# Kernel optimization log

Hardware: AMD Instinct MI355X
Metric: run time of the kernel (lower is better)

Reference implementation:

```python
import jax, jax.numpy as jnp
import numpy as np

T, B, D, H, DFF = 512, 32, 1024, 16, 4096
DK = D // H
SCALE = 1.0 / np.sqrt(DK)
EPS = 1e-5


def _layernorm(x, w, b):
    mu = jnp.mean(x, axis=-1, keepdims=True)
    var = jnp.mean(jnp.square(x - mu), axis=-1, keepdims=True)
    return (x - mu) * jax.lax.rsqrt(var + EPS) * w + b


def _gru_gate(x, y, wg, bg):
    # gates: (..., 3, D) from Linear(2D -> 3D, no bias)
    g = jnp.concatenate([x, y], axis=-1) @ wg.T
    g = g.reshape(*g.shape[:-1], 3, D)
    r = jax.nn.sigmoid(g[..., 0, :])
    z = jax.nn.sigmoid(g[..., 1, :] - bg)
    h = jnp.tanh(g[..., 2, :] * r)
    return (1 - z) * x + z * h


def _attention(x, w_qkv, w_out, b_out):
    t = x.shape[0]
    qkv = (x @ w_qkv.T).reshape(t, -1, 3, H, DK)  # (T,B,3,H,dk)
    q, k, v = qkv[:, :, 0], qkv[:, :, 1], qkv[:, :, 2]  # (T,B,H,dk)
    scores = jnp.einsum('tbhd,sbhd->bhts', q, k) * SCALE
    causal = jnp.triu(jnp.ones((t, t), dtype=bool), k=1)
    scores = jnp.where(causal, -jnp.inf, scores)
    attn = jax.nn.softmax(scores, axis=-1)
    out = jnp.einsum('bhts,sbhd->tbhd', attn, v).reshape(t, -1, D)
    return out @ w_out.T + b_out


def setup_inputs() -> dict:
    key = jax.random.key(0)
    ks = jax.random.split(key, 10)
    s = lambda k, shape, scale: jax.random.normal(k, shape, dtype=jnp.float32) * scale
    return {
        'x': s(ks[0], (T, B, D), 1.0),
        'w_qkv': s(ks[1], (3 * D, D), 0.02),
        'w_out': s(ks[2], (D, D), 0.02),
        'b_out': jnp.zeros((D,), jnp.float32),
        'ln1_w': jnp.ones((D,), jnp.float32),
        'ln1_b': jnp.zeros((D,), jnp.float32),
        'ln2_w': jnp.ones((D,), jnp.float32),
        'ln2_b': jnp.zeros((D,), jnp.float32),
        'w_ff1': s(ks[3], (DFF, D), 0.02),
        'b_ff1': jnp.zeros((DFF,), jnp.float32),
        'w_ff2': s(ks[4], (D, DFF), 0.02),
        'b_ff2': jnp.zeros((D,), jnp.float32),
        'g1_w': s(ks[5], (3 * D, 2 * D), 0.02),
        'g1_bg': jnp.full((D,), 2.0, jnp.float32),
        'g2_w': s(ks[6], (3 * D, 2 * D), 0.02),
        'g2_bg': jnp.full((D,), 2.0, jnp.float32),
    }


def reference(x, w_qkv, w_out, b_out, ln1_w, ln1_b, ln2_w, ln2_b,
              w_ff1, b_ff1, w_ff2, b_ff2, g1_w, g1_bg, g2_w, g2_bg):
    attn_out = _attention(_layernorm(x, ln1_w, ln1_b), w_qkv, w_out, b_out)
    h1 = _gru_gate(x, attn_out, g1_w, g1_bg)
    h = _layernorm(h1, ln2_w, ln2_b)
    ff = jax.nn.relu(h @ w_ff1.T + b_ff1) @ w_ff2.T + b_ff2
    return _gru_gate(h1, ff, g2_w, g2_bg)
```

## Files before the change

kernel.cpp:

```cpp
#include <hip/hip_runtime.h>

#define TT   512
#define BB   32
#define DD   1024
#define HH   16
#define NROW 16384

typedef __attribute__((ext_vector_type(4))) float f32x4;
typedef __attribute__((ext_vector_type(8))) short s16x8;
typedef __attribute__((ext_vector_type(4))) short s16x4;

__device__ __forceinline__ unsigned short f2bf(float f) {
    unsigned int u = __float_as_uint(f);
    u += 0x7fffu + ((u >> 16) & 1u);
    return (unsigned short)(u >> 16);
}
__device__ __forceinline__ float bf2f(unsigned short h) {
    return __uint_as_float(((unsigned int)h) << 16);
}

__device__ __forceinline__ void gload16(const unsigned short* g, unsigned short* l) {
    __builtin_amdgcn_global_load_lds(
        (const __attribute__((address_space(1))) unsigned int*)g,
        (__attribute__((address_space(3))) unsigned int*)l, 16, 0, 0);
}

__global__ __launch_bounds__(256, 8)
void fill_f32(float* __restrict__ p, float v) {
    const size_t i = ((size_t)blockIdx.x * 256 + threadIdx.x) * 4;
    f32x4 o = (f32x4){v, v, v, v};
    *(f32x4*)(p + i) = o;
}

__global__ __launch_bounds__(256, 8)
void cvt_weights(const float* __restrict__ s0, const float* __restrict__ s1,
                 const float* __restrict__ s2, const float* __restrict__ s3,
                 const float* __restrict__ s4, const float* __restrict__ s5,
                 unsigned short* __restrict__ dst) {
    const int i = blockIdx.x * 256 + threadIdx.x;
    const float* src;
    int base;
    if      (i <  786432) { src = s0; base = 0;       }
    else if (i < 1048576) { src = s1; base = 786432;  }
    else if (i < 2097152) { src = s2; base = 1048576; }
    else if (i < 3145728) { src = s3; base = 2097152; }
    else if (i < 4718592) { src = s4; base = 3145728; }
    else                  { src = s5; base = 4718592; }
    f32x4 v = *(const f32x4*)(src + (size_t)(i - base) * 4);
    s16x4 o;
#pragma unroll
    for (int j = 0; j < 4; ++j) o[j] = (short)f2bf(v[j]);
    *(s16x4*)(dst + (size_t)i * 4) = o;
}

__global__ __launch_bounds__(256, 8)
void cvt_rows(const float* __restrict__ in, unsigned short* __restrict__ out, int ld_out) {
    const int row = blockIdx.x;
    const int d   = threadIdx.x * 4;
    f32x4 v = *(const f32x4*)(in + (size_t)row * DD + d);
    s16x4 o;
#pragma unroll
    for (int j = 0; j < 4; ++j) o[j] = (short)f2bf(v[j]);
    *(s16x4*)(out + (size_t)row * ld_out + d) = o;
}

__global__ __launch_bounds__(256, 4)
void ln_fwd(const float* __restrict__ in, const float* __restrict__ w,
            const float* __restrict__ bsh, unsigned short* __restrict__ out,
            unsigned short* __restrict__ side, int ld_side) {
    const int row = blockIdx.x;
    const int tid = threadIdx.x;
    f32x4 v = *(const f32x4*)(in + (size_t)row * DD + tid * 4);
    float s = v[0] + v[1] + v[2] + v[3];
    float q = v[0]*v[0] + v[1]*v[1] + v[2]*v[2] + v[3]*v[3];
#pragma unroll
    for (int d = 1; d < 64; d <<= 1) {
        s += __shfl_xor(s, d, 64);
        q += __shfl_xor(q, d, 64);
    }
    __shared__ float red[8];
    const int lane = tid & 63, wv = tid >> 6;
    if (lane == 0) { red[wv] = s; red[4 + wv] = q; }
    __syncthreads();
    s = red[0] + red[1] + red[2] + red[3];
    q = red[4] + red[5] + red[6] + red[7];
    const float mu   = s * (1.f / 1024.f);
    const float rstd = rsqrtf(q * (1.f / 1024.f) - mu * mu + 1e-5f);
    f32x4 w4 = *(const f32x4*)(w + tid * 4);
    f32x4 b4 = *(const f32x4*)(bsh + tid * 4);
    s16x4 o;
#pragma unroll
    for (int j = 0; j < 4; ++j) o[j] = (short)f2bf((v[j] - mu) * rstd * w4[j] + b4[j]);
    *(s16x4*)(out + (size_t)row * DD + tid * 4) = o;
    if (side) {
        s16x4 sx;
#pragma unroll
        for (int j = 0; j < 4; ++j) sx[j] = (short)f2bf(v[j]);
        *(s16x4*)(side + (size_t)row * ld_side + tid * 4) = sx;
    }
}

__global__ __launch_bounds__(256, 2)
void gemm_bf16(const unsigned short* __restrict__ A,
               const unsigned short* __restrict__ W,
               unsigned short* __restrict__ C,
               const float* __restrict__ bias,
               int M, int N, int K, int ldc, int relu) {
    __shared__ unsigned short lds_a[128 * 64];
    __shared__ unsigned short lds_b[128 * 64];

    const int tid  = threadIdx.x;
    const int lane = tid & 63;
    const int wv   = tid >> 6;
    const int wm   = wv >> 1;
    const int wn   = wv & 1;
    const int m0   = blockIdx.y * 128;
    const int n0   = blockIdx.x * 128;
    const int l15  = lane & 15;
    const int l4   = lane >> 4;
    const int lrow   = lane >> 3;
    const int gchunk = (lane & 7) ^ lrow;

    f32x4 acc[4][4];
#pragma unroll
    for (int i = 0; i < 4; ++i)
#pragma unroll
        for (int j = 0; j < 4; ++j) acc[i][j] = (f32x4){0.f, 0.f, 0.f, 0.f};

    for (int k0 = 0; k0 < K; k0 += 64) {
        __syncthreads();
#pragma unroll
        for (int i = 0; i < 4; ++i) {
            const int r = (wv * 4 + i) * 8 + lrow;
            gload16(A + (size_t)(m0 + r) * K + k0 + gchunk * 8, lds_a + (wv * 4 + i) * 512);
            gload16(W + (size_t)(n0 + r) * K + k0 + gchunk * 8, lds_b + (wv * 4 + i) * 512);
        }
        __syncthreads();
#pragma unroll
        for (int ks = 0; ks < 2; ++ks) {
            s16x8 af[4], bfr[4];
#pragma unroll
            for (int mi = 0; mi < 4; ++mi) {
                const int row = wm * 64 + mi * 16 + l15;
                const int c   = ks * 4 + l4;
                af[mi] = *(const s16x8*)(lds_a + row * 64 + ((c ^ (row & 7)) * 8));
            }
#pragma unroll
            for (int ni = 0; ni < 4; ++ni) {
                const int row = wn * 64 + ni * 16 + l15;
                const int c   = ks * 4 + l4;
                bfr[ni] = *(const s16x8*)(lds_b + row * 64 + ((c ^ (row & 7)) * 8));
            }
#pragma unroll
            for (int mi = 0; mi < 4; ++mi)
#pragma unroll
                for (int ni = 0; ni < 4; ++ni)
                    acc[mi][ni] = __builtin_amdgcn_mfma_f32_16x16x32_bf16(
                        af[mi], bfr[ni], acc[mi][ni], 0, 0, 0);
        }
    }

    const int r0 = l4 * 4;
#pragma unroll
    for (int ni = 0; ni < 4; ++ni) {
        const int col = n0 + wn * 64 + ni * 16 + l15;
        const float bv = bias ? bias[col] : 0.f;
#pragma unroll
        for (int mi = 0; mi < 4; ++mi) {
            const int rowb = m0 + wm * 64 + mi * 16 + r0;
#pragma unroll
            for (int r = 0; r < 4; ++r) {
                float v = acc[mi][ni][r] + bv;
                if (relu) v = fmaxf(v, 0.f);
                C[(size_t)(rowb + r) * ldc + col] = f2bf(v);
            }
        }
    }
}

__global__ __launch_bounds__(256, 2)
void repack_qkv(const unsigned short* __restrict__ qkv,
                unsigned short* __restrict__ Qo, unsigned short* __restrict__ Ko,
                unsigned short* __restrict__ Vt) {
    __shared__ unsigned short vlds[64][65];
    const int tid = threadIdx.x;
    const int t0  = blockIdx.x * 64;
    const int bh  = blockIdx.y;
    const int b   = bh >> 4, h = bh & 15;
    {
        const int row = tid >> 2, ch = tid & 3;
        const int t = t0 + row;
        const unsigned short* src = qkv + (size_t)(t * BB + b) * 3072 + h * 64 + ch * 16;
        const size_t doff = ((size_t)bh * 512 + t) * 64 + ch * 16;
        *(s16x8*)(Qo + doff)     = *(const s16x8*)(src);
        *(s16x8*)(Qo + doff + 8) = *(const s16x8*)(src + 8);
        *(s16x8*)(Ko + doff)     = *(const s16x8*)(src + 1024);
        *(s16x8*)(Ko + doff + 8) = *(const s16x8*)(src + 1032);
    }
#pragma unroll
    for (int it = 0; it < 2; ++it) {
        const int vr = (tid >> 3) + it * 32;
        const int c8 = tid & 7;
        s16x8 val = *(const s16x8*)(qkv + (size_t)((t0 + vr) * BB + b) * 3072 + 2048 + h * 64 + c8 * 8);
#pragma unroll
        for (int j = 0; j < 8; ++j) vlds[vr][c8 * 8 + j] = (unsigned short)val[j];
    }
    __syncthreads();
    {
        const int dk = tid >> 2, ch = tid & 3;
        s16x8 o0, o1;
#pragma unroll
        for (int j = 0; j < 8; ++j) {
            o0[j] = (short)vlds[ch * 16 + j][dk];
            o1[j] = (short)vlds[ch * 16 + 8 + j][dk];
        }
        const size_t doff = ((size_t)bh * 64 + dk) * 512 + t0 + ch * 16;
        *(s16x8*)(Vt + doff)     = o0;
        *(s16x8*)(Vt + doff + 8) = o1;
    }
}

__global__ __launch_bounds__(256, 2)
void attn_fwd(const unsigned short* __restrict__ Qm,
              const unsigned short* __restrict__ Km,
              const unsigned short* __restrict__ Vt,
              unsigned short* __restrict__ Om) {
    __shared__ unsigned short lds_k[64 * 64];
    __shared__ unsigned short lds_v[64 * 64];
    __shared__ unsigned short p_lds[4][16 * 72];

    const int tid  = threadIdx.x;
    const int lane = tid & 63;
    const int wv   = tid >> 6;
    const int q0   = blockIdx.x * 64;
    const int bh   = blockIdx.y;
    const int b    = bh >> 4, h = bh & 15;
    const int l15  = lane & 15;
    const int l4   = lane >> 4;
    const int lrow   = lane >> 3;
    const int gchunk = (lane & 7) ^ lrow;

    s16x8 qa[2];
    {
        const unsigned short* qp = Qm + ((size_t)bh * 512 + q0 + wv * 16 + l15) * 64 + l4 * 8;
        qa[0] = *(const s16x8*)(qp);
        qa[1] = *(const s16x8*)(qp + 32);
    }

    f32x4 oacc[4];
#pragma unroll
    for (int i = 0; i < 4; ++i) oacc[i] = (f32x4){0.f, 0.f, 0.f, 0.f};
    float m_run[4], l_run[4];
#pragma unroll
    for (int r = 0; r < 4; ++r) { m_run[r] = -1e30f; l_run[r] = 0.f; }

    const int rowg0 = q0 + wv * 16 + l4 * 4;

    for (int s0 = 0; s0 <= q0; s0 += 64) {
        __syncthreads();
#pragma unroll
        for (int i = 0; i < 2; ++i) {
            const int r = (wv * 2 + i) * 8 + lrow;
            gload16(Km + ((size_t)bh * 512 + s0 + r) * 64 + gchunk * 8, lds_k + (wv * 2 + i) * 512);
            gload16(Vt + ((size_t)bh * 64 + r) * 512 + s0 + gchunk * 8, lds_v + (wv * 2 + i) * 512);
        }
        __syncthreads();

        float svv[4][4];
#pragma unroll
        for (int ni = 0; ni < 4; ++ni) {
            f32x4 s = (f32x4){0.f, 0.f, 0.f, 0.f};
#pragma unroll
            for (int ks = 0; ks < 2; ++ks) {
                const int row = ni * 16 + l15;
                const int c   = ks * 4 + l4;
                s16x8 kb = *(const s16x8*)(lds_k + row * 64 + ((c ^ (row & 7)) * 8));
                s = __builtin_amdgcn_mfma_f32_16x16x32_bf16(qa[ks], kb, s, 0, 0, 0);
            }
            const int colg = s0 + ni * 16 + l15;
#pragma unroll
            for (int r = 0; r < 4; ++r)
                svv[ni][r] = (colg > rowg0 + r) ? -1e30f : s[r] * 0.125f;
        }
#pragma unroll
        for (int r = 0; r < 4; ++r) {
            float mt = fmaxf(fmaxf(svv[0][r], svv[1][r]), fmaxf(svv[2][r], svv[3][r]));
            mt = fmaxf(mt, __shfl_xor(mt, 1, 64));
            mt = fmaxf(mt, __shfl_xor(mt, 2, 64));
            mt = fmaxf(mt, __shfl_xor(mt, 4, 64));
            mt = fmaxf(mt, __shfl_xor(mt, 8, 64));
            const float mn    = fmaxf(m_run[r], mt);
            const float alpha = __expf(m_run[r] - mn);
            m_run[r] = mn;
            float rs = 0.f;
#pragma unroll
            for (int ni = 0; ni < 4; ++ni) {
                const float p = __expf(svv[ni][r] - mn);
                svv[ni][r] = p;
                rs += p;
            }
            rs += __shfl_xor(rs, 1, 64);
            rs += __shfl_xor(rs, 2, 64);
            rs += __shfl_xor(rs, 4, 64);
            rs += __shfl_xor(rs, 8, 64);
            l_run[r] = l_run[r] * alpha + rs;
#pragma unroll
            for (int ni = 0; ni < 4; ++ni) oacc[ni][r] *= alpha;
        }
#pragma unroll
        for (int ni = 0; ni < 4; ++ni)
#pragma unroll
            for (int r = 0; r < 4; ++r)
                p_lds[wv][(l4 * 4 + r) * 72 + ni * 16 + l15] = f2bf(svv[ni][r]);
        __syncthreads();
        s16x8 pa[2];
        {
            const unsigned short* pp = &p_lds[wv][l15 * 72 + l4 * 8];
            pa[0] = *(const s16x8*)(pp);
            pa[1] = *(const s16x8*)(pp + 32);
        }
#pragma unroll
        for (int ni = 0; ni < 4; ++ni)
#pragma unroll
            for (int ks = 0; ks < 2; ++ks) {
                const int row = ni * 16 + l15;
                const int c   = ks * 4 + l4;
                s16x8 vb = *(const s16x8*)(lds_v + row * 64 + ((c ^ (row & 7)) * 8));
                oacc[ni] = __builtin_amdgcn_mfma_f32_16x16x32_bf16(pa[ks], vb, oacc[ni], 0, 0, 0);
            }
    }
#pragma unroll
    for (int ni = 0; ni < 4; ++ni)
#pragma unroll
        for (int r = 0; r < 4; ++r) {
            const int t = rowg0 + r;
            Om[((size_t)t * BB + b) * DD + h * 64 + ni * 16 + l15] = f2bf(oacc[ni][r] / l_run[r]);
        }
}

__global__ __launch_bounds__(256, 4)
void gru_gate_ln(const unsigned short* __restrict__ g, const float* xin,
                 const float* __restrict__ bg,
                 const float* __restrict__ lnw, const float* __restrict__ lnb,
                 float* outf,
                 unsigned short* __restrict__ side_bf, int ld_side,
                 unsigned short* __restrict__ lnout_bf) {
    const int row = blockIdx.x;
    const int tid = threadIdx.x;
    const int d   = tid * 4;
    const unsigned short* gp = g + (size_t)row * 3072 + d;
    s16x4 g0 = *(const s16x4*)(gp);
    s16x4 g1 = *(const s16x4*)(gp + 1024);
    s16x4 g2 = *(const s16x4*)(gp + 2048);
    f32x4 xv  = *(const f32x4*)(xin + (size_t)row * DD + d);
    f32x4 bgv = *(const f32x4*)(bg + d);
    f32x4 of;
    s16x4 ob;
#pragma unroll
    for (int j = 0; j < 4; ++j) {
        const float a0 = bf2f((unsigned short)g0[j]);
        const float a1 = bf2f((unsigned short)g1[j]);
        const float a2 = bf2f((unsigned short)g2[j]);
        const float r = 1.f / (1.f + __expf(-a0));
        const float z = 1.f / (1.f + __expf(-(a1 - bgv[j])));
        const float t = a2 * r;
        const float e = __expf(2.f * t);
        const float th = 1.f - 2.f / (e + 1.f);
        const float o = (1.f - z) * xv[j] + z * th;
        of[j] = o;
        ob[j] = (short)f2bf(o);
    }
    *(f32x4*)(outf + (size_t)row * DD + d) = of;
    if (side_bf) *(s16x4*)(side_bf + (size_t)row * ld_side + d) = ob;

    if (lnw) {
        float s = of[0] + of[1] + of[2] + of[3];
        float q = of[0]*of[0] + of[1]*of[1] + of[2]*of[2] + of[3]*of[3];
#pragma unroll
        for (int dd = 1; dd < 64; dd <<= 1) {
            s += __shfl_xor(s, dd, 64);
            q += __shfl_xor(q, dd, 64);
        }
        __shared__ float red[8];
        const int lane = tid & 63, wvi = tid >> 6;
        if (lane == 0) { red[wvi] = s; red[4 + wvi] = q; }
        __syncthreads();
        s = red[0] + red[1] + red[2] + red[3];
        q = red[4] + red[5] + red[6] + red[7];
        const float mu   = s * (1.f / 1024.f);
        const float rstd = rsqrtf(q * (1.f / 1024.f) - mu * mu + 1e-5f);
        f32x4 w4 = *(const f32x4*)(lnw + d);
        f32x4 b4 = *(const f32x4*)(lnb + d);
        s16x4 lo;
#pragma unroll
        for (int j = 0; j < 4; ++j) lo[j] = (short)f2bf((of[j] - mu) * rstd * w4[j] + b4[j]);
        *(s16x4*)(lnout_bf + (size_t)row * DD + d) = lo;
    }
}

extern "C" void kernel_launch(void* const* d_in, const int* in_sizes, int n_in,
                              void* d_out, int out_size, void* d_ws, size_t ws_size,
                              hipStream_t stream) {
    const float* x     = (const float*)d_in[0];
    const float* w_qkv = (const float*)d_in[1];
    const float* w_out = (const float*)d_in[2];
    const float* b_out = (const float*)d_in[3];
    const float* ln1_w = (const float*)d_in[4];
    const float* ln1_b = (const float*)d_in[5];
    const float* ln2_w = (const float*)d_in[6];
    const float* ln2_b = (const float*)d_in[7];
    const float* w_ff1 = (const float*)d_in[8];
    const float* b_ff1 = (const float*)d_in[9];
    const float* w_ff2 = (const float*)d_in[10];
    const float* b_ff2 = (const float*)d_in[11];
    const float* g1_w  = (const float*)d_in[12];
    const float* g1_bg = (const float*)d_in[13];
    const float* g2_w  = (const float*)d_in[14];
    const float* g2_bg = (const float*)d_in[15];

    float* out = (float*)d_out;

    if (ws_size < 176160768ULL) {
        fill_f32<<<16384, 256, 0, stream>>>(out, 1.0e6f);
        return;
    }

    char* ws = (char*)d_ws;
    unsigned short* wall  = (unsigned short*)(ws + 0);
    unsigned short* wq_b  = (unsigned short*)(ws + 0);
    unsigned short* wo_b  = (unsigned short*)(ws + 6291456);
    unsigned short* wf1_b = (unsigned short*)(ws + 8388608);
    unsigned short* wf2_b = (unsigned short*)(ws + 16777216);
    unsigned short* wg1_b = (unsigned short*)(ws + 25165824);
    unsigned short* wg2_b = (unsigned short*)(ws + 37748736);
    unsigned short* xn_bf  = (unsigned short*)(ws + 50331648);
    unsigned short* vT_bh  = xn_bf;
    unsigned short* qkv_bf = (unsigned short*)(ws + 83886080);
    unsigned short* aO_bf  = qkv_bf;
    unsigned short* xc   = (unsigned short*)(ws + 117440512);
    unsigned short* hbf  = (unsigned short*)(ws + 134217728);
    unsigned short* gbuf = (unsigned short*)(ws + 142606336);

    unsigned short* q_bh = (unsigned short*)d_out;
    unsigned short* k_bh = q_bh + 16777216;
    float*          h1   = out;

    cvt_weights<<<24576, 256, 0, stream>>>(w_qkv, w_out, w_ff1, w_ff2, g1_w, g2_w, wall);

    ln_fwd<<<NROW, 256, 0, stream>>>(x, ln1_w, ln1_b, xn_bf, nullptr, 0);

    gemm_bf16<<<dim3(24, 128), 256, 0, stream>>>(xn_bf, wq_b, qkv_bf, nullptr,
                                                 NROW, 3072, 1024, 3072, 0);
    repack_qkv<<<dim3(8, 512), 256, 0, stream>>>(qkv_bf, q_bh, k_bh, vT_bh);

    attn_fwd<<<dim3(8, 512), 256, 0, stream>>>(q_bh, k_bh, vT_bh, aO_bf);

    const int RCH = 4096;
    for (int c = 0; c < 4; ++c) {
        const int r0 = c * RCH;
        cvt_rows<<<RCH, 256, 0, stream>>>(x + (size_t)r0 * DD, xc, 2048);
        gemm_bf16<<<dim3(8, RCH / 128), 256, 0, stream>>>(
            aO_bf + (size_t)r0 * 1024, wo_b, xc + 1024, b_out, RCH, 1024, 1024, 2048, 0);
        gemm_bf16<<<dim3(24, RCH / 128), 256, 0, stream>>>(
            xc, wg1_b, gbuf, nullptr, RCH, 3072, 2048, 3072, 0);
        gru_gate_ln<<<RCH, 256, 0, stream>>>(gbuf, x + (size_t)r0 * DD, g1_bg,
                                             ln2_w, ln2_b, h1 + (size_t)r0 * DD,
                                             xc, 2048, hbf);
        gemm_bf16<<<dim3(32, RCH / 128), 256, 0, stream>>>(
            hbf, wf1_b, gbuf, b_ff1, RCH, 4096, 1024, 4096, 1);
        gemm_bf16<<<dim3(8, RCH / 128), 256, 0, stream>>>(
            gbuf, wf2_b, xc + 1024, b_ff2, RCH, 1024, 4096, 2048, 0);
        gemm_bf16<<<dim3(24, RCH / 128), 256, 0, stream>>>(
            xc, wg2_b, gbuf, nullptr, RCH, 3072, 2048, 3072, 0);
        gru_gate_ln<<<RCH, 256, 0, stream>>>(gbuf, h1 + (size_t)r0 * DD, g2_bg,
                                             nullptr, nullptr, h1 + (size_t)r0 * DD,
                                             nullptr, 0, nullptr);
    }
}
```

Before: 1.628 ms.

## Add 256x256-tile double-buffered GEMM kernel and route most projections to it

```diff
diff --git a/kernel.cpp b/kernel.cpp
--- a/kernel.cpp
+++ b/kernel.cpp
@@ -176,6 +176,112 @@
             }
         }
     }
+}
+
+__global__ __launch_bounds__(512, 2)
+void gemm256(const unsigned short* __restrict__ A,
+             const unsigned short* __restrict__ W,
+             unsigned short* __restrict__ C,
+             const float* __restrict__ bias,
+             int M, int N, int K, int lda, int ldc, int relu) {
+    __shared__ unsigned short lds[2][2][16384];
+
+    const int tid  = threadIdx.x;
+    const int lane = tid & 63;
+    const int w    = tid >> 6;
+    const int wm   = w >> 2;
+    const int wn   = w & 3;
+    const int l15  = lane & 15;
+    const int l4   = lane >> 4;
+    const int lrow = lane >> 3;
+    const int gch  = (lane & 7) ^ lrow;
+
+    const int nbn = N >> 8;
+    const int nwg = (M >> 8) * nbn;
+    int bid = blockIdx.x;
+    if ((nwg & 7) == 0) { const int cpx = nwg >> 3; bid = (bid & 7) * cpx + (bid >> 3); }
+    const int m0 = (bid / nbn) << 8;
+    const int n0 = (bid % nbn) << 8;
+
+    f32x4 acc[8][4];
+#pragma unroll
+    for (int i = 0; i < 8; ++i)
+#pragma unroll
+        for (int j = 0; j < 4; ++j) acc[i][j] = (f32x4){0.f, 0.f, 0.f, 0.f};
+
+    auto STAGE = [&](int p, int k0) {
+#pragma unroll
+        for (int i = 0; i < 4; ++i) {
+            const int s   = w * 4 + i;
+            const int row = s * 8 + lrow;
+            gload16(A + (size_t)(m0 + row) * lda + k0 + gch * 8, &lds[p][0][s * 512]);
+            gload16(W + (size_t)(n0 + row) * K   + k0 + gch * 8, &lds[p][1][s * 512]);
+        }
+    };
+
+    auto COMPUTE = [&](int p) {
+#pragma unroll
+        for (int kk = 0; kk < 2; ++kk) {
+            const int cc = kk * 4 + l4;
+            s16x8 bf[4];
+#pragma unroll
+            for (int fc = 0; fc < 4; ++fc) {
+                const int rowb = wn * 64 + fc * 16 + l15;
+                bf[fc] = *(const s16x8*)&lds[p][1][rowb * 64 + ((cc ^ (rowb & 7)) * 8)];
+            }
+#pragma unroll
+            for (int fr = 0; fr < 8; ++fr) {
+                const int rowa = wm * 128 + fr * 16 + l15;
+                s16x8 af = *(const s16x8*)&lds[p][0][rowa * 64 + ((cc ^ (rowa & 7)) * 8)];
+#pragma unroll
+                for (int fc = 0; fc < 4; ++fc)
+                    acc[fr][fc] = __builtin_amdgcn_mfma_f32_16x16x32_bf16(
+                        af, bf[fc], acc[fr][fc], 0, 0, 0);
+            }
+        }
+    };
+
+    const int nt = K >> 6;
+
+    STAGE(0, 0);
+    STAGE(1, 64);
+    asm volatile("s_waitcnt vmcnt(8)" ::: "memory");
+    __builtin_amdgcn_sched_barrier(0);
+    __builtin_amdgcn_s_barrier();
+    __builtin_amdgcn_sched_barrier(0);
+
+    int p = 0;
+    for (int t = 0; t < nt; ++t) {
+        COMPUTE(p);
+        asm volatile("s_waitcnt lgkmcnt(0)" ::: "memory");
+        __builtin_amdgcn_sched_barrier(0);
+        __builtin_amdgcn_s_barrier();
+        __builtin_amdgcn_sched_barrier(0);
+        if (t + 2 < nt) {
+            STAGE(p, (t + 2) * 64);
+            asm volatile("s_waitcnt vmcnt(8)" ::: "memory");
+        } else if (t + 1 < nt) {
+            asm volatile("s_waitcnt vmcnt(0)" ::: "memory");
+        }
+        __builtin_amdgcn_sched_barrier(0);
+        __builtin_amdgcn_s_barrier();
+        __builtin_amdgcn_sched_barrier(0);
+        p ^= 1;
+    }
+
+#pragma unroll
+    for (int fr = 0; fr < 8; ++fr)
+#pragma unroll
+        for (int fc = 0; fc < 4; ++fc) {
+            const int col = n0 + wn * 64 + fc * 16 + l15;
+            const float bv = bias ? bias[col] : 0.f;
+#pragma unroll
+            for (int r = 0; r < 4; ++r) {
+                float v = acc[fr][fc][r] + bv;
+                if (relu) v = fmaxf(v, 0.f);
+                C[(size_t)(m0 + wm * 128 + fr * 16 + l4 * 4 + r) * ldc + col] = f2bf(v);
+            }
+        }
 }
 
 __global__ __launch_bounds__(256, 2)
@@ -449,8 +555,8 @@
 
     ln_fwd<<<NROW, 256, 0, stream>>>(x, ln1_w, ln1_b, xn_bf, nullptr, 0);
 
-    gemm_bf16<<<dim3(24, 128), 256, 0, stream>>>(xn_bf, wq_b, qkv_bf, nullptr,
-                                                 NROW, 3072, 1024, 3072, 0);
+    gemm256<<<768, 512, 0, stream>>>(xn_bf, wq_b, qkv_bf, nullptr,
+                                     NROW, 3072, 1024, 1024, 3072, 0);
     repack_qkv<<<dim3(8, 512), 256, 0, stream>>>(qkv_bf, q_bh, k_bh, vT_bh);
 
     attn_fwd<<<dim3(8, 512), 256, 0, stream>>>(q_bh, k_bh, vT_bh, aO_bf);
@@ -459,19 +565,19 @@
     for (int c = 0; c < 4; ++c) {
         const int r0 = c * RCH;
         cvt_rows<<<RCH, 256, 0, stream>>>(x + (size_t)r0 * DD, xc, 2048);
-        gemm_bf16<<<dim3(8, RCH / 128), 256, 0, stream>>>(
-            aO_bf + (size_t)r0 * 1024, wo_b, xc + 1024, b_out, RCH, 1024, 1024, 2048, 0);
-        gemm_bf16<<<dim3(24, RCH / 128), 256, 0, stream>>>(
-            xc, wg1_b, gbuf, nullptr, RCH, 3072, 2048, 3072, 0);
+        gemm256<<<64, 512, 0, stream>>>(aO_bf + (size_t)r0 * 1024, wo_b, xc + 1024,
+                                        b_out, RCH, 1024, 1024, 1024, 2048, 0);
+        gemm256<<<192, 512, 0, stream>>>(xc, wg1_b, gbuf, nullptr,
+                                         RCH, 3072, 2048, 2048, 3072, 0);
         gru_gate_ln<<<RCH, 256, 0, stream>>>(gbuf, x + (size_t)r0 * DD, g1_bg,
                                              ln2_w, ln2_b, h1 + (size_t)r0 * DD,
                                              xc, 2048, hbf);
-        gemm_bf16<<<dim3(32, RCH / 128), 256, 0, stream>>>(
-            hbf, wf1_b, gbuf, b_ff1, RCH, 4096, 1024, 4096, 1);
+        gemm256<<<256, 512, 0, stream>>>(hbf, wf1_b, gbuf, b_ff1,
+                                         RCH, 4096, 1024, 1024, 4096, 1);
         gemm_bf16<<<dim3(8, RCH / 128), 256, 0, stream>>>(
             gbuf, wf2_b, xc + 1024, b_ff2, RCH, 1024, 4096, 2048, 0);
-        gemm_bf16<<<dim3(24, RCH / 128), 256, 0, stream>>>(
-            xc, wg2_b, gbuf, nullptr, RCH, 3072, 2048, 3072, 0);
+        gemm256<<<192, 512, 0, stream>>>(xc, wg2_b, gbuf, nullptr,
+                                         RCH, 3072, 2048, 2048, 3072, 0);
         gru_gate_ln<<<RCH, 256, 0, stream>>>(gbuf, h1 + (size_t)r0 * DD, g2_bg,
                                              nullptr, nullptr, h1 + (size_t)r0 * DD,
                                              nullptr, 0, nullptr);
```

New measurement: 1.727 ms. 1.06x slower.
